# Kernel tuning notes

Measured on AMD Instinct MI355X. Metric: run time of the kernel, lower is better.

## Reference

```python
import jax, jax.numpy as jnp
import numpy as np

T, D, E, F, K = 8192, 1024, 8, 2048, 2


def setup_inputs() -> dict:
    key = jax.random.key(0)
    ks = jax.random.split(key, 5)
    s_in = 1.0 / np.sqrt(D)
    s_mid = 1.0 / np.sqrt(F)
    return {
        "x": jax.random.normal(ks[0], (T, D), dtype=jnp.float32),
        "wg": jax.random.normal(ks[1], (D, E), dtype=jnp.float32) * s_in,
        "w1": jax.random.normal(ks[2], (E, D, F), dtype=jnp.float32) * s_in,
        "w3": jax.random.normal(ks[3], (E, D, F), dtype=jnp.float32) * s_in,
        "w2": jax.random.normal(ks[4], (E, F, D), dtype=jnp.float32) * s_mid,
    }


def reference(x, wg, w1, w3, w2):
    # Gating: top-k over expert logits, softmax over the selected k (fp32)
    gate_logits = x @ wg                      # [T, E]
    top_w, sel = jax.lax.top_k(gate_logits, K)  # [T, K]
    probs = jax.nn.softmax(top_w.astype(jnp.float32), axis=1).astype(x.dtype)
    # combine[t, e] = sum_k probs[t, k] * (sel[t, k] == e)
    combine = jnp.einsum("tk,tke->te", probs, jax.nn.one_hot(sel, E, dtype=x.dtype))
    # Dense expert evaluation (same math as the per-expert gather/scatter loop:
    # tokens with combine[t,e]==0 contribute nothing)
    h = jax.nn.silu(jnp.einsum("td,edf->tef", x, w1)) * jnp.einsum("td,edf->tef", x, w3)
    out = jnp.einsum("tef,efd,te->td", h, w2, combine)
    return out
```

## Files before the change

### kernel.cpp

```cpp
#include <hip/hip_runtime.h>
#include <stdint.h>

#define T_TOK 8192
#define DDIM 1024
#define EEXP 8
#define FDIM 2048
#define GBLK 512

typedef float f32x4 __attribute__((ext_vector_type(4)));
typedef __bf16 bf16x8 __attribute__((ext_vector_type(8)));
typedef unsigned short us8 __attribute__((ext_vector_type(8)));

#define VMCNT(N) asm volatile("s_waitcnt vmcnt(" #N ")" ::: "memory")
#define BAR() __builtin_amdgcn_s_barrier()

__device__ __forceinline__ unsigned short f2bf(float f) {
  union { float f; unsigned int u; } v; v.f = f;
  unsigned int r = (v.u + 0x7fffu + ((v.u >> 16) & 1u)) >> 16;
  return (unsigned short)r;
}

__device__ __forceinline__ void async_cp16(const void* g, void* l) {
  __builtin_amdgcn_global_load_lds(
      (const __attribute__((address_space(1))) unsigned int*)g,
      (__attribute__((address_space(3))) unsigned int*)l, 16, 0, 0);
}

__global__ __launch_bounds__(256) void transpose_cast3_kernel(
    const float* __restrict__ w1, const float* __restrict__ w3, const float* __restrict__ w2,
    unsigned short* __restrict__ w1t, unsigned short* __restrict__ w3t,
    unsigned short* __restrict__ w2t) {
  __shared__ float tile[64][65];
  const int z = blockIdx.z;
  const float* in;
  unsigned short* out;
  int R, C;
  if (z < 16) {
    R = DDIM; C = FDIM;
    const float* s = (z < 8) ? w1 : w3;
    unsigned short* o = (z < 8) ? w1t : w3t;
    in = s + (size_t)(z & 7) * R * C;
    out = o + (size_t)(z & 7) * R * C;
  } else {
    R = FDIM; C = DDIM;
    in = w2 + (size_t)(z & 7) * R * C;
    out = w2t + (size_t)(z & 7) * R * C;
  }
  const int c0 = blockIdx.x * 64;
  const int r0 = blockIdx.y * 64;
  if (c0 >= C || r0 >= R) return;
  const int t = threadIdx.x;
  const int pr = t >> 4;
  const int pc = (t & 15) * 4;
#pragma unroll
  for (int i = 0; i < 4; i++) {
    float4 v = *(const float4*)&in[(size_t)(r0 + pr + i * 16) * C + c0 + pc];
    tile[pr + i * 16][pc + 0] = v.x;
    tile[pr + i * 16][pc + 1] = v.y;
    tile[pr + i * 16][pc + 2] = v.z;
    tile[pr + i * 16][pc + 3] = v.w;
  }
  __syncthreads();
  const int qr = (t & 7) * 8;
  const int qc = t >> 3;
#pragma unroll
  for (int i = 0; i < 2; i++) {
    int cc = qc + i * 32;
    us8 o;
#pragma unroll
    for (int j = 0; j < 8; j++) o[j] = f2bf(tile[qr + j][cc]);
    *(us8*)&out[(size_t)(c0 + cc) * R + r0 + qr] = o;
  }
}

__global__ __launch_bounds__(256) void gate_kernel(const float* __restrict__ x,
                                                   const float* __restrict__ wg,
                                                   unsigned short* __restrict__ xb,
                                                   int* __restrict__ sel,
                                                   float* __restrict__ prb,
                                                   int* __restrict__ cnt_blk) {
  __shared__ float wgs[8 * 1024];
  __shared__ int cnt[8];
  const int tid = threadIdx.x;
  if (tid < 8) cnt[tid] = 0;
  for (int i = tid; i < 8192; i += 256) {
    int d = i >> 3, e = i & 7;
    wgs[e * 1024 + d] = wg[i];
  }
  __syncthreads();
  const int lane = tid & 63;
  const int wv = tid >> 6;
#pragma unroll 1
  for (int tt = 0; tt < 4; tt++) {
    const int t = blockIdx.x * 16 + tt * 4 + wv;
    const float4* xp = (const float4*)(x + (size_t)t * 1024);
    float4 xv[4];
#pragma unroll
    for (int it = 0; it < 4; it++) xv[it] = xp[lane + it * 64];
    float acc[8] = {0.f, 0.f, 0.f, 0.f, 0.f, 0.f, 0.f, 0.f};
    ushort4* xbp = (ushort4*)(xb + (size_t)t * 1024);
#pragma unroll
    for (int it = 0; it < 4; it++) {
      const int d = (lane + it * 64) * 4;
      float4 v = xv[it];
      ushort4 o;
      o.x = f2bf(v.x); o.y = f2bf(v.y); o.z = f2bf(v.z); o.w = f2bf(v.w);
      xbp[lane + it * 64] = o;
#pragma unroll
      for (int e = 0; e < 8; e++)
        acc[e] += v.x * wgs[e * 1024 + d] + v.y * wgs[e * 1024 + d + 1] +
                  v.z * wgs[e * 1024 + d + 2] + v.w * wgs[e * 1024 + d + 3];
    }
#pragma unroll
    for (int e = 0; e < 8; e++) {
      acc[e] += __shfl_xor(acc[e], 32);
      acc[e] += __shfl_xor(acc[e], 16);
      acc[e] += __shfl_xor(acc[e], 8);
      acc[e] += __shfl_xor(acc[e], 4);
      acc[e] += __shfl_xor(acc[e], 2);
      acc[e] += __shfl_xor(acc[e], 1);
    }
    if (lane == 0) {
      int i0 = 0; float v0 = acc[0];
#pragma unroll
      for (int e = 1; e < 8; e++) if (acc[e] > v0) { v0 = acc[e]; i0 = e; }
      int i1 = -1; float v1 = -1e30f;
#pragma unroll
      for (int e = 0; e < 8; e++) if (e != i0 && acc[e] > v1) { v1 = acc[e]; i1 = e; }
      float ex = __expf(v1 - v0);
      float inv = 1.0f / (1.0f + ex);
      sel[t * 2] = i0; sel[t * 2 + 1] = i1;
      prb[t * 2] = inv; prb[t * 2 + 1] = ex * inv;
      atomicAdd(&cnt[i0], 1);
      atomicAdd(&cnt[i1], 1);
    }
  }
  __syncthreads();
  if (tid < 8) cnt_blk[blockIdx.x * 8 + tid] = cnt[tid];
}

__global__ __launch_bounds__(64) void scan_kernel(const int* __restrict__ cnt_blk,
                                                  int* __restrict__ hdr,
                                                  int* __restrict__ blk_off) {
  __shared__ int part[64];
  const int i = threadIdx.x;
  const int e = i & 7, chunk = i >> 3;
  const int CPB = GBLK / 8;
  int s = 0;
  for (int b = 0; b < CPB; b++) s += cnt_blk[(chunk * CPB + b) * 8 + e];
  part[i] = s;
  __syncthreads();
  if (i < 8) {
    int tot = 0;
#pragma unroll
    for (int c = 0; c < 8; c++) tot += part[c * 8 + i];
    hdr[i] = tot;
  }
  __syncthreads();
  if (i == 0) {
    int s2 = 0;
    for (int e2 = 0; e2 < 8; e2++) { hdr[16 + e2] = s2; s2 += hdr[e2]; }
    hdr[24] = s2;
  }
  __syncthreads();
  int running = hdr[16 + e];
  for (int c = 0; c < chunk; c++) running += part[c * 8 + e];
  for (int b = 0; b < CPB; b++) {
    int idx = (chunk * CPB + b) * 8 + e;
    blk_off[idx] = running;
    running += cnt_blk[idx];
  }
}

__global__ __launch_bounds__(64) void build_kernel(const int* __restrict__ sel,
                                                   const int* __restrict__ blk_off,
                                                   int* __restrict__ rows,
                                                   int* __restrict__ slot_of) {
  const int lane = threadIdx.x;
  const int i = blockIdx.x * 64 + lane;
  const int gb = i >> 5;
  const int e = sel[i];
  unsigned long long m = 0;
#pragma unroll
  for (int ee = 0; ee < 8; ee++) {
    unsigned long long be = __ballot(e == ee);
    if (ee == e) m = be;
  }
  const unsigned long long half =
      (lane < 32) ? 0x00000000FFFFFFFFull : 0xFFFFFFFF00000000ull;
  const unsigned long long below = (1ull << lane) - 1ull;
  const int rank = __popcll(m & half & below);
  const int pos = blk_off[gb * 8 + e] + rank;
  rows[pos] = i >> 1;
  slot_of[i] = pos;
}


__global__ __launch_bounds__(512, 2) void gemm1_kernel(
    const unsigned short* __restrict__ xb,
    const unsigned short* __restrict__ w1t,
    const unsigned short* __restrict__ w3t,
    const int* __restrict__ rows,
    const int* __restrict__ hdr,
    unsigned short* __restrict__ h)
{
  const int e = blockIdx.z;
  const int count = hdr[e];
  const int m0 = blockIdx.y * 256;
  if (m0 >= count) return;
  const int n0 = blockIdx.x * 128;
  const int sbase = hdr[16 + e];

  __shared__ unsigned short As[2][16384];
  __shared__ unsigned short Bs[2][16384];

  const int tid = threadIdx.x;
  const int srcoff = ((tid & 7) ^ ((tid >> 3) & 7)) * 8;
  const int rq = tid >> 3;
  const unsigned short* pA[4];
#pragma unroll
  for (int q = 0; q < 4; q++) {
    int m = m0 + q * 64 + rq; if (m > count - 1) m = count - 1;
    pA[q] = xb + (size_t)rows[sbase + m] * DDIM + srcoff;
  }
  const unsigned short* pB[4];
  pB[0] = w1t + ((size_t)e * FDIM + n0 + rq) * DDIM + srcoff;
  pB[1] = w1t + ((size_t)e * FDIM + n0 + 64 + rq) * DDIM + srcoff;
  pB[2] = w3t + ((size_t)e * FDIM + n0 + rq) * DDIM + srcoff;
  pB[3] = w3t + ((size_t)e * FDIM + n0 + 64 + rq) * DDIM + srcoff;
  const int l0 = tid * 8;

  const int wv = tid >> 6;
  const int wr = (wv >> 2) * 128;
  const int wn = (wv & 3) * 32;
  const int lane = tid & 63;
  const int lm = lane & 15;
  const int ls = lane >> 4;
  const int coff0 = ((ls) ^ (lm & 7)) * 8;
  const int coff1 = ((4 + ls) ^ (lm & 7)) * 8;

  f32x4 acc1[8][2], acc3[8][2];
#pragma unroll
  for (int i = 0; i < 8; i++)
#pragma unroll
    for (int j = 0; j < 2; j++) {
      acc1[i][j] = f32x4{0.f, 0.f, 0.f, 0.f};
      acc3[i][j] = f32x4{0.f, 0.f, 0.f, 0.f};
    }

  bf16x8 a[8], b1[4], b3[4];

  auto stageA0 = [&](int buf, int kt) {
    async_cp16(pA[0] + kt, &As[buf][l0]);
    async_cp16(pA[2] + kt, &As[buf][8192 + l0]);
  };
  auto stageA1 = [&](int buf, int kt) {
    async_cp16(pA[1] + kt, &As[buf][4096 + l0]);
    async_cp16(pA[3] + kt, &As[buf][12288 + l0]);
  };
  auto stageB0 = [&](int buf, int kt) {
    async_cp16(pB[0] + kt, &Bs[buf][l0]);
    async_cp16(pB[1] + kt, &Bs[buf][4096 + l0]);
  };
  auto stageB1 = [&](int buf, int kt) {
    async_cp16(pB[2] + kt, &Bs[buf][8192 + l0]);
    async_cp16(pB[3] + kt, &Bs[buf][12288 + l0]);
  };
  auto rdA = [&](int cur, int mh) {
#pragma unroll
    for (int i = 0; i < 4; i++) {
      const unsigned short* rp = &As[cur][(wr + mh * 64 + i * 16 + lm) * 64];
      a[i * 2 + 0] = *(const bf16x8*)(rp + coff0);
      a[i * 2 + 1] = *(const bf16x8*)(rp + coff1);
    }
  };
  auto rdB = [&](int cur, int half, bf16x8* bb) {
#pragma unroll
    for (int j = 0; j < 2; j++) {
      const unsigned short* rp = &Bs[cur][(half * 128 + wn + j * 16 + lm) * 64];
      bb[j * 2 + 0] = *(const bf16x8*)(rp + coff0);
      bb[j * 2 + 1] = *(const bf16x8*)(rp + coff1);
    }
  };
  auto mm = [&](f32x4 (*acc)[2], int mh, bf16x8* bb) {
    __builtin_amdgcn_s_setprio(1);
#pragma unroll
    for (int i = 0; i < 4; i++)
#pragma unroll
      for (int j = 0; j < 2; j++) {
        f32x4 c = acc[mh * 4 + i][j];
        c = __builtin_amdgcn_mfma_f32_16x16x32_bf16(a[i * 2 + 0], bb[j * 2 + 0], c, 0, 0, 0);
        c = __builtin_amdgcn_mfma_f32_16x16x32_bf16(a[i * 2 + 1], bb[j * 2 + 1], c, 0, 0, 0);
        acc[mh * 4 + i][j] = c;
      }
    __builtin_amdgcn_s_setprio(0);
  };

  stageA0(0, 0); stageB0(0, 0); stageB1(0, 0); stageA1(0, 0);

  for (int t = 0; t < 15; ++t) {
    const int cur = t & 1, nxt = cur ^ 1;
    const int kt = (t + 1) * 64;
    stageA0(nxt, kt); VMCNT(6); BAR();
    rdA(cur, 0); rdB(cur, 0, b1); mm(acc1, 0, b1);
    stageB0(nxt, kt); VMCNT(6); BAR();
    rdB(cur, 1, b3); mm(acc3, 0, b3);
    stageB1(nxt, kt); VMCNT(6); BAR();
    rdA(cur, 1); mm(acc1, 1, b1);
    stageA1(nxt, kt); BAR();
    mm(acc3, 1, b3);
  }
  {
    VMCNT(4); BAR(); rdA(1, 0); rdB(1, 0, b1); mm(acc1, 0, b1);
    VMCNT(2); BAR(); rdB(1, 1, b3); mm(acc3, 0, b3);
    VMCNT(0); BAR(); rdA(1, 1); mm(acc1, 1, b1);
    BAR(); mm(acc3, 1, b3);
  }

#pragma unroll
  for (int i = 0; i < 8; i++) {
#pragma unroll
    for (int r = 0; r < 4; r++) {
      int mg = m0 + wr + i * 16 + ls * 4 + r;
      if (mg < count) {
        unsigned short* hp = h + (size_t)(sbase + mg) * FDIM + n0 + wn + lm;
#pragma unroll
        for (int j = 0; j < 2; j++) {
          float v1 = acc1[i][j][r];
          float v3 = acc3[i][j][r];
          float hv = (v1 / (1.0f + __expf(-v1))) * v3;
          hp[j * 16] = f2bf(hv);
        }
      }
    }
  }
}

__global__ __launch_bounds__(512, 2) void gemm2_kernel(
    const unsigned short* __restrict__ h,
    const unsigned short* __restrict__ w2t,
    const int* __restrict__ hdr,
    float* __restrict__ y)
{
  const int e = blockIdx.z;
  const int count = hdr[e];
  const int m0 = blockIdx.y * 256;
  if (m0 >= count) return;
  const int n0 = blockIdx.x * 256;
  const int sbase = hdr[16 + e];

  __shared__ unsigned short As[2][16384];
  __shared__ unsigned short Bs[2][16384];

  const int tid = threadIdx.x;
  const int srcoff = ((tid & 7) ^ ((tid >> 3) & 7)) * 8;
  const int rq = tid >> 3;
  const unsigned short* pA[4];
#pragma unroll
  for (int q = 0; q < 4; q++) {
    int m = m0 + q * 64 + rq; if (m > count - 1) m = count - 1;
    pA[q] = h + (size_t)(sbase + m) * FDIM + srcoff;
  }
  const unsigned short* pB[4];
#pragma unroll
  for (int q = 0; q < 4; q++)
    pB[q] = w2t + ((size_t)e * DDIM + n0 + q * 64 + rq) * FDIM + srcoff;
  const int l0 = tid * 8;

  const int wv = tid >> 6;
  const int wr = (wv >> 2) * 128;
  const int wn = (wv & 3) * 64;
  const int lane = tid & 63;
  const int lm = lane & 15;
  const int ls = lane >> 4;
  const int coff0 = ((ls) ^ (lm & 7)) * 8;
  const int coff1 = ((4 + ls) ^ (lm & 7)) * 8;

  f32x4 acc[8][4];
#pragma unroll
  for (int i = 0; i < 8; i++)
#pragma unroll
    for (int j = 0; j < 4; j++) acc[i][j] = f32x4{0.f, 0.f, 0.f, 0.f};

  bf16x8 a[8], b[8];

  auto stageA0 = [&](int buf, int kt) {
    async_cp16(pA[0] + kt, &As[buf][l0]);
    async_cp16(pA[2] + kt, &As[buf][8192 + l0]);
  };
  auto stageA1 = [&](int buf, int kt) {
    async_cp16(pA[1] + kt, &As[buf][4096 + l0]);
    async_cp16(pA[3] + kt, &As[buf][12288 + l0]);
  };
  auto stageB0 = [&](int buf, int kt) {
    async_cp16(pB[0] + kt, &Bs[buf][l0]);
    async_cp16(pB[1] + kt, &Bs[buf][4096 + l0]);
  };
  auto stageB1 = [&](int buf, int kt) {
    async_cp16(pB[2] + kt, &Bs[buf][8192 + l0]);
    async_cp16(pB[3] + kt, &Bs[buf][12288 + l0]);
  };
  auto rdA2 = [&](int cur, int mh, int kk) {
#pragma unroll
    for (int i = 0; i < 4; i++) {
      const unsigned short* rp = &As[cur][(wr + mh * 64 + i * 16 + lm) * 64];
      a[kk * 4 + i] = *(const bf16x8*)(rp + (kk ? coff1 : coff0));
    }
  };
  auto rdB2 = [&](int cur, int kk) {
#pragma unroll
    for (int j = 0; j < 4; j++) {
      const unsigned short* rp = &Bs[cur][(wn + j * 16 + lm) * 64];
      b[kk * 4 + j] = *(const bf16x8*)(rp + (kk ? coff1 : coff0));
    }
  };
  auto mm2 = [&](int mh, int kk) {
    __builtin_amdgcn_s_setprio(1);
#pragma unroll
    for (int i = 0; i < 4; i++)
#pragma unroll
      for (int j = 0; j < 4; j++)
        acc[mh * 4 + i][j] =
            __builtin_amdgcn_mfma_f32_16x16x32_bf16(a[kk * 4 + i], b[kk * 4 + j],
                                                    acc[mh * 4 + i][j], 0, 0, 0);
    __builtin_amdgcn_s_setprio(0);
  };

  stageB0(0, 0); stageB1(0, 0); stageA0(0, 0); stageA1(0, 0);

  for (int t = 0; t < 31; ++t) {
    const int cur = t & 1, nxt = cur ^ 1;
    const int kt = (t + 1) * 64;
    stageB0(nxt, kt); VMCNT(4); BAR();
    rdA2(cur, 0, 0); rdB2(cur, 0); mm2(0, 0);
    stageB1(nxt, kt); BAR();
    rdA2(cur, 0, 1); rdB2(cur, 1); mm2(0, 1);
    stageA0(nxt, kt); VMCNT(6); BAR();
    rdA2(cur, 1, 0); mm2(1, 0);
    stageA1(nxt, kt); BAR();
    rdA2(cur, 1, 1); mm2(1, 1);
  }
  {
    VMCNT(2); BAR(); rdA2(1, 0, 0); rdB2(1, 0); mm2(0, 0);
    BAR(); rdA2(1, 0, 1); rdB2(1, 1); mm2(0, 1);
    VMCNT(0); BAR(); rdA2(1, 1, 0); mm2(1, 0);
    BAR(); rdA2(1, 1, 1); mm2(1, 1);
  }

#pragma unroll
  for (int i = 0; i < 8; i++) {
#pragma unroll
    for (int r = 0; r < 4; r++) {
      int mg = m0 + wr + i * 16 + ls * 4 + r;
      if (mg < count) {
        float* yp = y + (size_t)(sbase + mg) * DDIM + n0 + wn + lm;
#pragma unroll
        for (int j = 0; j < 4; j++) yp[j * 16] = acc[i][j][r];
      }
    }
  }
}

__global__ __launch_bounds__(256) void combine_kernel(const float* __restrict__ y,
                                                      const int* __restrict__ slot_of,
                                                      const float* __restrict__ prb,
                                                      float* __restrict__ out) {
  int t = blockIdx.x;
  int s0 = slot_of[t * 2], s1 = slot_of[t * 2 + 1];
  float p0 = prb[t * 2], p1 = prb[t * 2 + 1];
  float4 a = ((const float4*)(y + (size_t)s0 * DDIM))[threadIdx.x];
  float4 b = ((const float4*)(y + (size_t)s1 * DDIM))[threadIdx.x];
  float4 o;
  o.x = p0 * a.x + p1 * b.x;
  o.y = p0 * a.y + p1 * b.y;
  o.z = p0 * a.z + p1 * b.z;
  o.w = p0 * a.w + p1 * b.w;
  ((float4*)(out + (size_t)t * DDIM))[threadIdx.x] = o;
}

extern "C" void kernel_launch(void* const* d_in, const int* in_sizes, int n_in,
                              void* d_out, int out_size, void* d_ws, size_t ws_size,
                              hipStream_t stream) {
  const float* x  = (const float*)d_in[0];
  const float* wg = (const float*)d_in[1];
  const float* w1 = (const float*)d_in[2];
  const float* w3 = (const float*)d_in[3];
  const float* w2 = (const float*)d_in[4];
  float* out = (float*)d_out;
  char* ws = (char*)d_ws;

  size_t off = 0;
  int* hdr = (int*)(ws + off); off += 256;
  int* sel = (int*)(ws + off); off += (size_t)T_TOK * 2 * 4;
  float* prb = (float*)(ws + off); off += (size_t)T_TOK * 2 * 4;
  int* rows = (int*)(ws + off); off += (size_t)T_TOK * 2 * 4;
  int* slot_of = (int*)(ws + off); off += (size_t)T_TOK * 2 * 4;
  int* cnt_blk = (int*)(ws + off); off += (size_t)GBLK * 8 * 4;
  int* blk_off = (int*)(ws + off); off += (size_t)GBLK * 8 * 4;
  unsigned short* xb  = (unsigned short*)(ws + off); off += (size_t)T_TOK * DDIM * 2;
  unsigned short* w1t = (unsigned short*)(ws + off); off += (size_t)EEXP * DDIM * FDIM * 2;
  unsigned short* w3t = (unsigned short*)(ws + off); off += (size_t)EEXP * DDIM * FDIM * 2;
  unsigned short* w2t = (unsigned short*)(ws + off); off += (size_t)EEXP * DDIM * FDIM * 2;
  unsigned short* h   = (unsigned short*)(ws + off); off += (size_t)T_TOK * 2 * FDIM * 2;
  float* y = (float*)w1t;

  gate_kernel<<<GBLK, 256, 0, stream>>>(x, wg, xb, sel, prb, cnt_blk);
  transpose_cast3_kernel<<<dim3(32, 32, 24), 256, 0, stream>>>(w1, w3, w2, w1t, w3t, w2t);
  scan_kernel<<<1, 64, 0, stream>>>(cnt_blk, hdr, blk_off);
  build_kernel<<<T_TOK * 2 / 64, 64, 0, stream>>>(sel, blk_off, rows, slot_of);
  gemm1_kernel<<<dim3(FDIM / 128, T_TOK / 128 / 2, EEXP), 512, 0, stream>>>(xb, w1t, w3t, rows, hdr, h);
  gemm2_kernel<<<dim3(DDIM / 256, T_TOK / 128 / 2, EEXP), 512, 0, stream>>>(h, w2t, hdr, y);
  combine_kernel<<<T_TOK, 256, 0, stream>>>(y, slot_of, prb, out);
}
```

Baseline: 568.4 us.

## Reschedule GEMM main loops into ping-pong phases with scheduling barriers

Restructures the K-loops of both expert GEMM kernels so that LDS reads and the next-tile async global-to-LDS copies are issued together in one phase, and the MFMA block runs alone in the next phase. Each phase is split by an s_barrier plus sched_barrier so the compiler cannot move instructions across them. The vmcnt wait points are also reworked. The aim is to keep memory traffic and matrix math in separate phases across waves and overlap them better. In exchange it adds twice as many workgroup barriers per iteration, and the LDS buffer reuse ordering has to be re-verified.

```diff
diff --git a/kernel.cpp b/kernel.cpp
--- a/kernel.cpp
+++ b/kernel.cpp
@@ -12,7 +12,7 @@
 typedef unsigned short us8 __attribute__((ext_vector_type(8)));
 
 #define VMCNT(N) asm volatile("s_waitcnt vmcnt(" #N ")" ::: "memory")
-#define BAR() __builtin_amdgcn_s_barrier()
+#define BARS() do { __builtin_amdgcn_s_barrier(); __builtin_amdgcn_sched_barrier(0); } while (0)
 
 __device__ __forceinline__ unsigned short f2bf(float f) {
   union { float f; unsigned int u; } v; v.f = f;
@@ -297,24 +297,28 @@
   };
 
   stageA0(0, 0); stageB0(0, 0); stageB1(0, 0); stageA1(0, 0);
+  VMCNT(4); BARS();
 
   for (int t = 0; t < 15; ++t) {
     const int cur = t & 1, nxt = cur ^ 1;
     const int kt = (t + 1) * 64;
-    stageA0(nxt, kt); VMCNT(6); BAR();
-    rdA(cur, 0); rdB(cur, 0, b1); mm(acc1, 0, b1);
-    stageB0(nxt, kt); VMCNT(6); BAR();
-    rdB(cur, 1, b3); mm(acc3, 0, b3);
-    stageB1(nxt, kt); VMCNT(6); BAR();
-    rdA(cur, 1); mm(acc1, 1, b1);
-    stageA1(nxt, kt); BAR();
+    rdA(cur, 0); rdB(cur, 0, b1); stageA0(nxt, kt); VMCNT(4); BARS();
+    mm(acc1, 0, b1); BARS();
+    rdB(cur, 1, b3); stageB0(nxt, kt); VMCNT(4); BARS();
+    mm(acc3, 0, b3); BARS();
+    rdA(cur, 1); stageB1(nxt, kt); BARS();
+    mm(acc1, 1, b1); BARS();
+    stageA1(nxt, kt); VMCNT(4); BARS();
+    mm(acc3, 1, b3); BARS();
+  }
+  {
+    rdA(1, 0); rdB(1, 0, b1); VMCNT(2); BARS();
+    mm(acc1, 0, b1); BARS();
+    rdB(1, 1, b3); VMCNT(0); BARS();
+    mm(acc3, 0, b3); BARS();
+    rdA(1, 1); BARS();
+    mm(acc1, 1, b1); BARS();
     mm(acc3, 1, b3);
-  }
-  {
-    VMCNT(4); BAR(); rdA(1, 0); rdB(1, 0, b1); mm(acc1, 0, b1);
-    VMCNT(2); BAR(); rdB(1, 1, b3); mm(acc3, 0, b3);
-    VMCNT(0); BAR(); rdA(1, 1); mm(acc1, 1, b1);
-    BAR(); mm(acc3, 1, b3);
   }
 
 #pragma unroll
@@ -427,24 +431,29 @@
   };
 
   stageB0(0, 0); stageB1(0, 0); stageA0(0, 0); stageA1(0, 0);
+  VMCNT(2); BARS();
 
   for (int t = 0; t < 31; ++t) {
     const int cur = t & 1, nxt = cur ^ 1;
     const int kt = (t + 1) * 64;
-    stageB0(nxt, kt); VMCNT(4); BAR();
-    rdA2(cur, 0, 0); rdB2(cur, 0); mm2(0, 0);
-    stageB1(nxt, kt); BAR();
-    rdA2(cur, 0, 1); rdB2(cur, 1); mm2(0, 1);
-    stageA0(nxt, kt); VMCNT(6); BAR();
-    rdA2(cur, 1, 0); mm2(1, 0);
-    stageA1(nxt, kt); BAR();
-    rdA2(cur, 1, 1); mm2(1, 1);
+    rdA2(cur, 0, 0); rdB2(cur, 0); stageB0(nxt, kt); BARS();
+    mm2(0, 0); BARS();
+    rdA2(cur, 0, 1); rdB2(cur, 1); stageB1(nxt, kt); VMCNT(4); BARS();
+    mm2(0, 1); BARS();
+    rdA2(cur, 1, 0); stageA0(nxt, kt); BARS();
+    mm2(1, 0); BARS();
+    rdA2(cur, 1, 1); stageA1(nxt, kt); VMCNT(2); BARS();
+    mm2(1, 1); BARS();
   }
   {
-    VMCNT(2); BAR(); rdA2(1, 0, 0); rdB2(1, 0); mm2(0, 0);
-    BAR(); rdA2(1, 0, 1); rdB2(1, 1); mm2(0, 1);
-    VMCNT(0); BAR(); rdA2(1, 1, 0); mm2(1, 0);
-    BAR(); rdA2(1, 1, 1); mm2(1, 1);
+    rdA2(1, 0, 0); rdB2(1, 0); BARS();
+    mm2(0, 0); BARS();
+    rdA2(1, 0, 1); rdB2(1, 1); VMCNT(0); BARS();
+    mm2(0, 1); BARS();
+    rdA2(1, 1, 0); BARS();
+    mm2(1, 0); BARS();
+    rdA2(1, 1, 1); BARS();
+    mm2(1, 1);
   }
 
 #pragma unroll
```

After: 560.5 us. Within noise of the previous version (-1.4%).

## Reorder LDS reads ahead of async stage issue in both expert GEMM pipelines

Applied to the files above, without the earlier changes.

In both grouped GEMM kernels (gate/up and down projections), each phase now issues its LDS fragment reads and the next async global-to-LDS stage before waiting at the barrier. The MFMA block then runs after the barrier. A prologue wait and barrier is added before the loop, the vmcnt thresholds are retuned, and the epilogue drops most of its barriers. The aim is to hide LDS read latency and cut barrier stalls between the MMA blocks. The risk is a hazard between the async writes into the next buffer and the reads of the current one if the wait counts are wrong.

```diff
diff --git a/kernel.cpp b/kernel.cpp
--- a/kernel.cpp
+++ b/kernel.cpp
@@ -297,24 +297,26 @@
   };
 
   stageA0(0, 0); stageB0(0, 0); stageB1(0, 0); stageA1(0, 0);
+  VMCNT(4); BAR();
 
   for (int t = 0; t < 15; ++t) {
     const int cur = t & 1, nxt = cur ^ 1;
     const int kt = (t + 1) * 64;
-    stageA0(nxt, kt); VMCNT(6); BAR();
-    rdA(cur, 0); rdB(cur, 0, b1); mm(acc1, 0, b1);
-    stageB0(nxt, kt); VMCNT(6); BAR();
-    rdB(cur, 1, b3); mm(acc3, 0, b3);
-    stageB1(nxt, kt); VMCNT(6); BAR();
-    rdA(cur, 1); mm(acc1, 1, b1);
-    stageA1(nxt, kt); BAR();
+    rdA(cur, 0); rdB(cur, 0, b1); stageA0(nxt, kt); VMCNT(4); BAR();
+    mm(acc1, 0, b1);
+    rdB(cur, 1, b3); stageB0(nxt, kt); VMCNT(4); BAR();
+    mm(acc3, 0, b3);
+    rdA(cur, 1); stageB1(nxt, kt); BAR();
+    mm(acc1, 1, b1);
+    stageA1(nxt, kt); VMCNT(4); BAR();
     mm(acc3, 1, b3);
   }
   {
-    VMCNT(4); BAR(); rdA(1, 0); rdB(1, 0, b1); mm(acc1, 0, b1);
-    VMCNT(2); BAR(); rdB(1, 1, b3); mm(acc3, 0, b3);
-    VMCNT(0); BAR(); rdA(1, 1); mm(acc1, 1, b1);
-    BAR(); mm(acc3, 1, b3);
+    rdA(1, 0); rdB(1, 0, b1); VMCNT(0); BAR();
+    mm(acc1, 0, b1);
+    rdB(1, 1, b3); mm(acc3, 0, b3);
+    rdA(1, 1); mm(acc1, 1, b1);
+    mm(acc3, 1, b3);
   }
 
 #pragma unroll
@@ -427,24 +429,26 @@
   };
 
   stageB0(0, 0); stageB1(0, 0); stageA0(0, 0); stageA1(0, 0);
+  VMCNT(2); BAR();
 
   for (int t = 0; t < 31; ++t) {
     const int cur = t & 1, nxt = cur ^ 1;
     const int kt = (t + 1) * 64;
-    stageB0(nxt, kt); VMCNT(4); BAR();
-    rdA2(cur, 0, 0); rdB2(cur, 0); mm2(0, 0);
-    stageB1(nxt, kt); BAR();
-    rdA2(cur, 0, 1); rdB2(cur, 1); mm2(0, 1);
-    stageA0(nxt, kt); VMCNT(6); BAR();
-    rdA2(cur, 1, 0); mm2(1, 0);
-    stageA1(nxt, kt); BAR();
-    rdA2(cur, 1, 1); mm2(1, 1);
+    rdA2(cur, 0, 0); rdB2(cur, 0); stageB0(nxt, kt); BAR();
+    mm2(0, 0);
+    rdA2(cur, 0, 1); rdB2(cur, 1); stageB1(nxt, kt); VMCNT(4); BAR();
+    mm2(0, 1);
+    rdA2(cur, 1, 0); stageA0(nxt, kt); BAR();
+    mm2(1, 0);
+    rdA2(cur, 1, 1); stageA1(nxt, kt); VMCNT(2); BAR();
+    mm2(1, 1);
   }
   {
-    VMCNT(2); BAR(); rdA2(1, 0, 0); rdB2(1, 0); mm2(0, 0);
-    BAR(); rdA2(1, 0, 1); rdB2(1, 1); mm2(0, 1);
-    VMCNT(0); BAR(); rdA2(1, 1, 0); mm2(1, 0);
-    BAR(); rdA2(1, 1, 1); mm2(1, 1);
+    rdA2(1, 0, 0); rdB2(1, 0); VMCNT(0); BAR();
+    mm2(0, 0);
+    rdA2(1, 0, 1); rdB2(1, 1); mm2(0, 1);
+    rdA2(1, 1, 0); mm2(1, 0);
+    rdA2(1, 1, 1); mm2(1, 1);
   }
 
 #pragma unroll
```

Measured after the change: 542.4 us. 1.05x faster.
